# Kernel optimization log

Measured on AMD Instinct MI355X. Metric: run time of the kernel, lower is better.

The kernel has to match this reference:

```python
import jax, jax.numpy as jnp
import numpy as np

B, S, E, H = 1, 2048, 4096, 32
D = E // H
MAX_POS = 2048
NEG_MASK = -66504.0
SCALE = float(np.sqrt(D))


def _rope(x, position_ids):
    # x: [B, S, H, D]; GPT-NeoX style rotate-half rotary embedding
    half = D // 2
    inv_freq = 1.0 / (10000.0 ** (jnp.arange(0, half, dtype=jnp.float32) * 2.0 / D))  # [D/2]
    ang = position_ids.astype(jnp.float32)[:, None] * inv_freq[None, :]               # [S, D/2]
    cos = jnp.cos(ang)[None, :, None, :]
    sin = jnp.sin(ang)[None, :, None, :]
    x1, x2 = x[..., :half], x[..., half:]
    return jnp.concatenate([x1 * cos - x2 * sin, x2 * cos + x1 * sin], axis=-1)


def setup_inputs() -> dict:
    key = jax.random.key(0)
    ks = jax.random.split(key, 9)
    s = 0.02
    return {
        "hidden_states": jax.random.normal(ks[0], (B, S, E), jnp.float32),
        "wq": jax.random.normal(ks[1], (E, E), jnp.float32) * s,
        "bq": jnp.zeros((E,), jnp.float32),
        "wk": jax.random.normal(ks[2], (E, E), jnp.float32) * s,
        "bk": jnp.zeros((E,), jnp.float32),
        "wv": jax.random.normal(ks[3], (E, E), jnp.float32) * s,
        "bv": jnp.zeros((E,), jnp.float32),
        "wo": jax.random.normal(ks[4], (E, E), jnp.float32) * s,
        "bo": jnp.zeros((E,), jnp.float32),
        "position_ids": jnp.arange(S, dtype=jnp.int32),
    }


def reference(hidden_states, wq, bq, wk, bk, wv, bv, wo, bo, position_ids):
    # QKV projections (nn.Linear: x @ W.T + b)
    q = hidden_states @ wq.T + bq
    k = hidden_states @ wk.T + bk
    v = hidden_states @ wv.T + bv
    # [B, S, H, D]
    q = q.reshape(B, S, H, D)
    k = k.reshape(B, S, H, D)
    v = v.reshape(B, S, H, D)
    # rotary embedding on key and query
    q = _rope(q, position_ids)
    k = _rope(k, position_ids)
    # [B, H, S, D]
    q = q.transpose(0, 2, 1, 3)
    k = k.transpose(0, 2, 1, 3)
    v = v.transpose(0, 2, 1, 3)
    # attention scores; causal mask added BEFORE dividing by scale (faithful to source)
    scores = jnp.einsum("bhqd,bhkd->bhqk", q, k)
    causal = (1.0 - jnp.tril(jnp.ones((S, S), jnp.float32))) * NEG_MASK  # [S, S]
    scores = (scores + causal[None, None]) / SCALE
    attn = jax.nn.softmax(scores.astype(jnp.float32), axis=-1).astype(q.dtype)
    ctx = jnp.einsum("bhqk,bhkd->bhqd", attn, v)
    ctx = ctx.transpose(0, 2, 1, 3).reshape(B, S, E)
    return ctx @ wo.T + bo
```

## Files before the change

### kernel.cpp

```cpp
#include <hip/hip_runtime.h>
#include <hip/hip_bf16.h>

constexpr int SEQ = 2048;
constexpr int EMB = 4096;
constexpr int NH  = 32;
constexpr int HD  = 128;
constexpr int HALF = 64;

typedef __bf16 bf16x8 __attribute__((ext_vector_type(8)));
typedef float  f32x4  __attribute__((ext_vector_type(4)));
using u16 = unsigned short;
typedef u16 ushort8 __attribute__((ext_vector_type(8)));
typedef u16 u16x4 __attribute__((ext_vector_type(4)));

__device__ inline float bf2f(u16 u) {
  union { unsigned int i; float f; } v; v.i = ((unsigned int)u) << 16; return v.f;
}
__device__ inline u16 f2bf(float f) {
  union { __bf16 b; u16 u; } v; v.b = (__bf16)f; return v.u;
}

#define GLL16(gp, lp) __builtin_amdgcn_global_load_lds( \
    (const __attribute__((address_space(1))) void*)(gp), \
    (__attribute__((address_space(3))) void*)(lp), 16, 0, 0)

__global__ void k_f32_to_bf16(const float* __restrict__ in, u16* __restrict__ out, int n) {
  int i = (blockIdx.x * blockDim.x + threadIdx.x) * 8;
  if (i >= n) return;
  f32x4 a = *(const f32x4*)(in + i);
  f32x4 b = *(const f32x4*)(in + i + 4);
  ushort8 o;
  o[0] = f2bf(a[0]); o[1] = f2bf(a[1]); o[2] = f2bf(a[2]); o[3] = f2bf(a[3]);
  o[4] = f2bf(b[0]); o[5] = f2bf(b[1]); o[6] = f2bf(b[2]); o[7] = f2bf(b[3]);
  *(ushort8*)(out + i) = o;
}

__global__ void k_rope_table(const int* __restrict__ pos, float* __restrict__ tab) {
  int idx = blockIdx.x * blockDim.x + threadIdx.x;
  if (idx >= SEQ * HALF) return;
  int s = idx >> 6, d = idx & 63;
  double invf = pow(10000.0, -(double)d / 64.0);
  double ang = (double)pos[s] * invf;
  tab[idx * 2]     = (float)cos(ang);
  tab[idx * 2 + 1] = (float)sin(ang);
}

__global__ void k_rope(u16* __restrict__ X, const float* __restrict__ tab, float scale) {
  int idx = blockIdx.x * blockDim.x + threadIdx.x;
  if (idx >= SEQ * NH * HALF) return;
  int d = idx & 63;
  int h = (idx >> 6) & 31;
  int s = idx >> 11;
  u16* p = X + (size_t)s * EMB + h * HD + d;
  float x1 = bf2f(p[0]), x2 = bf2f(p[HALF]);
  float c  = tab[(s * HALF + d) * 2];
  float sn = tab[(s * HALF + d) * 2 + 1];
  p[0]    = f2bf((x1 * c - x2 * sn) * scale);
  p[HALF] = f2bf((x2 * c + x1 * sn) * scale);
}

template<int TBM, int TBN, int WM, int WN>
__global__ __launch_bounds__(WM * WN * 64) void k_gemm(
    const u16* __restrict__ A, const u16* __restrict__ W,
    const float* __restrict__ b0, const float* __restrict__ b1, const float* __restrict__ b2,
    void* __restrict__ C0, void* __restrict__ C1, void* __restrict__ C2,
    int M, int N, int K, int mode)
{
  constexpr int CH_A = TBM / 16, CH_B = TBN / 16;
  constexpr int CH_W = (CH_A + CH_B) / (WM * WN);
  constexpr int MA = TBM / WM / 16, NB = TBN / WN / 16;
  __shared__ alignas(16) u16 As[2][TBM * 32];
  __shared__ alignas(16) u16 Bs[2][TBN * 32];
  int tid = threadIdx.x;
  int lane = tid & 63, wid = tid >> 6;
  int wm = wid / WN, wn = wid % WN;
  int l15 = lane & 15, lhi = lane >> 4;

  int NBY = M / TBM, NBX = N / TBN;
  int wg = blockIdx.x;
  int xcd = wg & 7, s = wg >> 3;
  int by = s % NBY, bxl = s / NBY;
  int bx = xcd * (NBX >> 3) + bxl;
  int m0 = by * TBM, n0 = bx * TBN;

  f32x4 acc[MA][NB] = {};

  int srow = lane >> 2;
  int scol = (lane & 3) * 8;

  auto stage = [&](int buf, int k0) {
#pragma unroll
    for (int i = 0; i < CH_W; i++) {
      int chunk = wid * CH_W + i;
      if (chunk < CH_A) {
        int row = chunk * 16 + srow;
        GLL16(A + (size_t)(m0 + row) * K + k0 + scol, &As[buf][chunk * 512]);
      } else {
        int c2 = chunk - CH_A;
        int row = c2 * 16 + srow;
        GLL16(W + (size_t)(n0 + row) * K + k0 + scol, &Bs[buf][c2 * 512]);
      }
    }
  };

  int KT = K / 32;
  stage(0, 0);
  for (int t = 0; t < KT; t++) {
    __syncthreads();
    if (t + 1 < KT) stage((t + 1) & 1, (t + 1) * 32);

    const u16* as = As[t & 1];
    const u16* bs = Bs[t & 1];
    bf16x8 af[MA], bfr[NB];
#pragma unroll
    for (int a = 0; a < MA; a++)
      af[a] = *(const bf16x8*)&as[(wm * (TBM / WM) + a * 16 + l15) * 32 + lhi * 8];
#pragma unroll
    for (int b = 0; b < NB; b++)
      bfr[b] = *(const bf16x8*)&bs[(wn * (TBN / WN) + b * 16 + l15) * 32 + lhi * 8];
#pragma unroll
    for (int a = 0; a < MA; a++)
#pragma unroll
      for (int b = 0; b < NB; b++)
        acc[a][b] = __builtin_amdgcn_mfma_f32_16x16x32_bf16(af[a], bfr[b], acc[a][b], 0, 0, 0);
  }

  const float* bias = b0;
  void* Cout = C0;
  int mode_l = mode, Nn = N, n_base = n0;
  if (mode == 3) {
    int seg = n0 >> 12;
    Nn = EMB; n_base = n0 & 4095;
    if (seg == 0)      { bias = b0; Cout = C0; mode_l = 0; }
    else if (seg == 1) { bias = b1; Cout = C1; mode_l = 0; }
    else               { bias = b2; Cout = C2; mode_l = 2; }
  }

#pragma unroll
  for (int a = 0; a < MA; a++) {
    int m = m0 + wm * (TBM / WM) + a * 16 + lhi * 4;
#pragma unroll
    for (int b = 0; b < NB; b++) {
      int n = n_base + wn * (TBN / WN) + b * 16 + l15;
      float bs2 = bias[n];
      if (mode_l == 2) {
        u16x4 pk;
#pragma unroll
        for (int r = 0; r < 4; r++) pk[r] = f2bf(acc[a][b][r] + bs2);
        *(u16x4*)&((u16*)Cout)[(size_t)n * M + m] = pk;
      } else if (mode_l == 1) {
#pragma unroll
        for (int r = 0; r < 4; r++)
          ((float*)Cout)[(size_t)(m + r) * Nn + n] = acc[a][b][r] + bs2;
      } else {
#pragma unroll
        for (int r = 0; r < 4; r++)
          ((u16*)Cout)[(size_t)(m + r) * Nn + n] = f2bf(acc[a][b][r] + bs2);
      }
    }
  }
}

constexpr int QB = 64, KVB = 64;

__global__ __launch_bounds__(256) void k_flash(
    const u16* __restrict__ Q, const u16* __restrict__ K, const u16* __restrict__ VT,
    u16* __restrict__ ctx)
{
  __shared__ alignas(16) u16 Ks[2][KVB * 128];
  __shared__ alignas(16) u16 Vt[2][HD * 64];
  __shared__ alignas(16) u16 Pl[4][16 * 64];

  int tid = threadIdx.x, lane = tid & 63, wid = tid >> 6;
  int l15 = lane & 15, lhi = lane >> 4;
  int h = blockIdx.y;

  auto stage = [&](int buf, int t2) {
    int kv = t2 * KVB;
#pragma unroll
    for (int it = 0; it < 4; it++) {
      int chunk = tid + it * 256;
      int r = chunk >> 4, bp = chunk & 15;
      GLL16(K + (size_t)(kv + r) * EMB + h * HD + (((bp - r) & 15) << 3), &Ks[buf][chunk * 8]);
    }
#pragma unroll
    for (int it = 0; it < 4; it++) {
      int chunk = tid + it * 256;
      int d = chunk >> 3, bp = chunk & 7;
      GLL16(VT + (size_t)(h * HD + d) * SEQ + kv + (((bp - d) & 7) << 3), &Vt[buf][chunk * 8]);
    }
  };

  for (int pi = 0; pi < 2; pi++) {
    int qb = pi ? (int)blockIdx.x : 31 - (int)blockIdx.x;
    int q0 = qb * QB;
    int qw = q0 + wid * 16;

    bf16x8 qf[4];
#pragma unroll
    for (int kc = 0; kc < 4; kc++)
      qf[kc] = *(const bf16x8*)&Q[(size_t)(qw + l15) * EMB + h * HD + kc * 32 + lhi * 8];

    f32x4 O[8] = {};
    float mrow[4], lrow[4];
#pragma unroll
    for (int r = 0; r < 4; r++) { mrow[r] = -3.0e38f; lrow[r] = 0.f; }

    int nt = qb + 1;
    __syncthreads();
    stage(0, 0);
    for (int t = 0; t < nt; t++) {
      __syncthreads();
      if (t + 1 < nt) stage((t + 1) & 1, t + 1);

      const u16* ks = Ks[t & 1];
      const u16* vt = Vt[t & 1];
      float p[4][4];
      bool need_mask = (t == nt - 1);
#pragma unroll
      for (int c = 0; c < 4; c++) {
        f32x4 s = {};
        int r0 = c * 16 + l15;
#pragma unroll
        for (int kc = 0; kc < 4; kc++) {
          bf16x8 kf = *(const bf16x8*)&ks[r0 * 128 + (((kc * 4 + lhi) + r0) & 15) * 8];
          s = __builtin_amdgcn_mfma_f32_16x16x32_bf16(qf[kc], kf, s, 0, 0, 0);
        }
#pragma unroll
        for (int r = 0; r < 4; r++) {
          float sv = s[r];
          if (need_mask) {
            int qg = qw + lhi * 4 + r;
            int kg = t * KVB + c * 16 + l15;
            if (kg > qg) sv = -3.0e38f;
          }
          p[c][r] = sv;
        }
      }
      float fscale[4];
#pragma unroll
      for (int r = 0; r < 4; r++) {
        float m = fmaxf(fmaxf(p[0][r], p[1][r]), fmaxf(p[2][r], p[3][r]));
#pragma unroll
        for (int x = 1; x < 16; x <<= 1) m = fmaxf(m, __shfl_xor(m, x, 64));
        float mnew = fmaxf(mrow[r], m);
        fscale[r] = __expf(mrow[r] - mnew);
        mrow[r] = mnew;
      }
#pragma unroll
      for (int c = 0; c < 4; c++)
#pragma unroll
        for (int r = 0; r < 4; r++)
          p[c][r] = __expf(p[c][r] - mrow[r]);
#pragma unroll
      for (int r = 0; r < 4; r++) {
        float s = p[0][r] + p[1][r] + p[2][r] + p[3][r];
#pragma unroll
        for (int x = 1; x < 16; x <<= 1) s += __shfl_xor(s, x, 64);
        lrow[r] = lrow[r] * fscale[r] + s;
      }
#pragma unroll
      for (int d = 0; d < 8; d++)
#pragma unroll
        for (int r = 0; r < 4; r++)
          O[d][r] *= fscale[r];
#pragma unroll
      for (int c = 0; c < 4; c++) {
        int kb = c * 2 + (l15 >> 3), klo = l15 & 7;
#pragma unroll
        for (int r = 0; r < 4; r++) {
          int q = lhi * 4 + r;
          Pl[wid][q * 64 + ((kb + (q >> 1)) & 7) * 8 + klo] = f2bf(p[c][r]);
        }
      }
#pragma unroll
      for (int ks2 = 0; ks2 < 2; ks2++) {
        int kb = ks2 * 4 + lhi;
        bf16x8 pf = *(const bf16x8*)&Pl[wid][l15 * 64 + ((kb + (l15 >> 1)) & 7) * 8];
#pragma unroll
        for (int ds = 0; ds < 8; ds++) {
          int d = ds * 16 + l15;
          bf16x8 vf = *(const bf16x8*)&vt[d * 64 + ((kb + d) & 7) * 8];
          O[ds] = __builtin_amdgcn_mfma_f32_16x16x32_bf16(pf, vf, O[ds], 0, 0, 0);
        }
      }
    }

#pragma unroll
    for (int r = 0; r < 4; r++) {
      float inv = 1.f / lrow[r];
      int qg = q0 + wid * 16 + lhi * 4 + r;
#pragma unroll
      for (int ds = 0; ds < 8; ds++)
        ctx[(size_t)qg * EMB + h * HD + ds * 16 + l15] = f2bf(O[ds][r] * inv);
    }
  }
}

extern "C" void kernel_launch(void* const* d_in, const int* in_sizes, int n_in,
                              void* d_out, int out_size, void* d_ws, size_t ws_size,
                              hipStream_t stream) {
  const float* hs = (const float*)d_in[0];
  const float* wq = (const float*)d_in[1];
  const float* bq = (const float*)d_in[2];
  const float* wk = (const float*)d_in[3];
  const float* bk = (const float*)d_in[4];
  const float* wv = (const float*)d_in[5];
  const float* bv = (const float*)d_in[6];
  const float* wo = (const float*)d_in[7];
  const float* bo = (const float*)d_in[8];
  const int*  pos = (const int*)d_in[9];

  const size_t SE = (size_t)SEQ * EMB;
  const size_t EE = (size_t)EMB * EMB;
  const float qscale = 1.0f / 11.313708498984761f;

  char* ws = (char*)d_ws;
  size_t off = 0;
  auto alloc = [&](size_t b) { size_t o = off; off += (b + 255) & ~(size_t)255; return o; };

  size_t need_fused = ((SE * 2 + 255) & ~255ULL) + ((EE * 6 + 255) & ~255ULL) +
                      3 * ((SE * 2 + 255) & ~255ULL) + ((size_t)SEQ * HALF * 8 + 255);
  bool fused = ws_size >= need_fused + 4096;

  u16*  hsb = (u16*)(ws + alloc(SE * 2));
  u16*  wb  = (u16*)(ws + alloc(fused ? EE * 6 : EE * 2));
  u16*  Qb  = (u16*)(ws + alloc(SE * 2));
  u16*  Kb  = (u16*)(ws + alloc(SE * 2));
  u16*  VTb = (u16*)(ws + alloc(SE * 2));
  float* tab = (float*)(ws + alloc((size_t)SEQ * HALF * 2 * 4));
  u16*  ctxb = hsb;

  dim3 cb(256);
  k_f32_to_bf16<<<dim3(SE / 2048), cb, 0, stream>>>(hs, hsb, (int)SE);
  k_rope_table<<<dim3(SEQ * HALF / 256), cb, 0, stream>>>(pos, tab);

  if (fused) {
    k_f32_to_bf16<<<dim3(EE / 2048), cb, 0, stream>>>(wq, wb, (int)EE);
    k_f32_to_bf16<<<dim3(EE / 2048), cb, 0, stream>>>(wk, wb + EE, (int)EE);
    k_f32_to_bf16<<<dim3(EE / 2048), cb, 0, stream>>>(wv, wb + 2 * EE, (int)EE);
    k_gemm<128, 256, 2, 4><<<dim3(768), dim3(512), 0, stream>>>(
        hsb, wb, bq, bk, bv, (void*)Qb, (void*)Kb, (void*)VTb, SEQ, 3 * EMB, EMB, 3);
  } else {
    k_f32_to_bf16<<<dim3(EE / 2048), cb, 0, stream>>>(wq, wb, (int)EE);
    k_gemm<128, 256, 2, 4><<<dim3(256), dim3(512), 0, stream>>>(
        hsb, wb, bq, bq, bq, (void*)Qb, nullptr, nullptr, SEQ, EMB, EMB, 0);
    k_f32_to_bf16<<<dim3(EE / 2048), cb, 0, stream>>>(wk, wb, (int)EE);
    k_gemm<128, 256, 2, 4><<<dim3(256), dim3(512), 0, stream>>>(
        hsb, wb, bk, bk, bk, (void*)Kb, nullptr, nullptr, SEQ, EMB, EMB, 0);
    k_f32_to_bf16<<<dim3(EE / 2048), cb, 0, stream>>>(wv, wb, (int)EE);
    k_gemm<128, 256, 2, 4><<<dim3(256), dim3(512), 0, stream>>>(
        hsb, wb, bv, bv, bv, (void*)VTb, nullptr, nullptr, SEQ, EMB, EMB, 2);
  }

  k_rope<<<dim3(SEQ * NH * HALF / 256), cb, 0, stream>>>(Qb, tab, qscale);
  k_rope<<<dim3(SEQ * NH * HALF / 256), cb, 0, stream>>>(Kb, tab, 1.0f);

  k_flash<<<dim3(16, NH), cb, 0, stream>>>(Qb, Kb, VTb, ctxb);

  k_f32_to_bf16<<<dim3(EE / 2048), cb, 0, stream>>>(wo, wb, (int)EE);
  k_gemm<64, 128, 2, 2><<<dim3(1024), cb, 0, stream>>>(
      ctxb, wb, bo, bo, bo, d_out, nullptr, nullptr, SEQ, EMB, EMB, 1);
}
```

Measured before the change: 553.5 us.

## Replace templated GEMM with triple-buffered swizzled 128x256 BK64 kernel

Swaps the double-buffered BK=32 templated GEMM for a dedicated 128x256 tile kernel with BK=64, a three-stage LDS ring and explicit vmcnt waits. The next-next stage loads are interleaved with the MFMA sub-steps. LDS rows are XOR-style swizzled to avoid bank conflicts, and s_setprio is raised around the MFMA bursts. The output projection now also uses the large tile, at 256 workgroups instead of 1024, trading occupancy and wave count for more data reuse and fewer barriers.

```diff
diff --git a/kernel.cpp b/kernel.cpp
--- a/kernel.cpp
+++ b/kernel.cpp
@@ -59,70 +59,94 @@
   p[HALF] = f2bf((x2 * c + x1 * sn) * scale);
 }
 
-template<int TBM, int TBN, int WM, int WN>
-__global__ __launch_bounds__(WM * WN * 64) void k_gemm(
-    const u16* __restrict__ A, const u16* __restrict__ W,
+__global__ __launch_bounds__(512) void k_gemm8(
+    const u16* __restrict__ Ag, const u16* __restrict__ Wg,
     const float* __restrict__ b0, const float* __restrict__ b1, const float* __restrict__ b2,
     void* __restrict__ C0, void* __restrict__ C1, void* __restrict__ C2,
     int M, int N, int K, int mode)
 {
-  constexpr int CH_A = TBM / 16, CH_B = TBN / 16;
-  constexpr int CH_W = (CH_A + CH_B) / (WM * WN);
-  constexpr int MA = TBM / WM / 16, NB = TBN / WN / 16;
-  __shared__ alignas(16) u16 As[2][TBM * 32];
-  __shared__ alignas(16) u16 Bs[2][TBN * 32];
+  __shared__ alignas(16) u16 As[3][128 * 64];
+  __shared__ alignas(16) u16 Bs[3][256 * 64];
+
   int tid = threadIdx.x;
   int lane = tid & 63, wid = tid >> 6;
-  int wm = wid / WN, wn = wid % WN;
+  int wm = wid >> 2, wn = wid & 3;
   int l15 = lane & 15, lhi = lane >> 4;
 
-  int NBY = M / TBM, NBX = N / TBN;
+  int NBY = M / 128, NBX = N / 256;
   int wg = blockIdx.x;
-  int xcd = wg & 7, s = wg >> 3;
-  int by = s % NBY, bxl = s / NBY;
+  int xcd = wg & 7, sgl = wg >> 3;
+  int by = sgl % NBY, bxl = sgl / NBY;
   int bx = xcd * (NBX >> 3) + bxl;
-  int m0 = by * TBM, n0 = bx * TBN;
-
-  f32x4 acc[MA][NB] = {};
-
-  int srow = lane >> 2;
-  int scol = (lane & 3) * 8;
-
-  auto stage = [&](int buf, int k0) {
-#pragma unroll
-    for (int i = 0; i < CH_W; i++) {
-      int chunk = wid * CH_W + i;
-      if (chunk < CH_A) {
-        int row = chunk * 16 + srow;
-        GLL16(A + (size_t)(m0 + row) * K + k0 + scol, &As[buf][chunk * 512]);
-      } else {
-        int c2 = chunk - CH_A;
-        int row = c2 * 16 + srow;
-        GLL16(W + (size_t)(n0 + row) * K + k0 + scol, &Bs[buf][c2 * 512]);
-      }
+  int m0 = by * 128, n0 = bx * 256;
+
+  auto stageA = [&](int b, int k0) {
+#pragma unroll
+    for (int s2 = 0; s2 < 2; s2++) {
+      int row = s2 * 64 + (tid >> 3);
+      int kb = ((tid & 7) - row) & 7;
+      GLL16(Ag + (size_t)(m0 + row) * K + k0 + kb * 8, &As[b][s2 * 4096 + tid * 8]);
     }
   };
-
-  int KT = K / 32;
-  stage(0, 0);
+  auto stageBh = [&](int b, int k0, int h) {
+#pragma unroll
+    for (int s2 = 0; s2 < 2; s2++) {
+      int row = h * 128 + s2 * 64 + (tid >> 3);
+      int kb = ((tid & 7) - row) & 7;
+      GLL16(Wg + (size_t)(n0 + row) * K + k0 + kb * 8, &Bs[b][h * 8192 + s2 * 4096 + tid * 8]);
+    }
+  };
+
+  f32x4 acc[4][4] = {};
+  int KT = K >> 6;
+
+  stageA(0, 0);  stageBh(0, 0, 0);  stageBh(0, 0, 1);
+  stageA(1, 64); stageBh(1, 64, 0); stageBh(1, 64, 1);
+
   for (int t = 0; t < KT; t++) {
-    __syncthreads();
-    if (t + 1 < KT) stage((t + 1) & 1, (t + 1) * 32);
-
-    const u16* as = As[t & 1];
-    const u16* bs = Bs[t & 1];
-    bf16x8 af[MA], bfr[NB];
-#pragma unroll
-    for (int a = 0; a < MA; a++)
-      af[a] = *(const bf16x8*)&as[(wm * (TBM / WM) + a * 16 + l15) * 32 + lhi * 8];
-#pragma unroll
-    for (int b = 0; b < NB; b++)
-      bfr[b] = *(const bf16x8*)&bs[(wn * (TBN / WN) + b * 16 + l15) * 32 + lhi * 8];
-#pragma unroll
-    for (int a = 0; a < MA; a++)
-#pragma unroll
-      for (int b = 0; b < NB; b++)
-        acc[a][b] = __builtin_amdgcn_mfma_f32_16x16x32_bf16(af[a], bfr[b], acc[a][b], 0, 0, 0);
+    if (t + 1 < KT) asm volatile("s_waitcnt vmcnt(6)" ::: "memory");
+    else            asm volatile("s_waitcnt vmcnt(0)" ::: "memory");
+    __builtin_amdgcn_s_barrier();
+
+    const u16* as = &As[t % 3][0];
+    const u16* bs = &Bs[t % 3][0];
+    bool do_stage = (t + 2) < KT;
+    int bstage = (t + 2) % 3;
+    int ks = (t + 2) << 6;
+
+    bf16x8 bfr[4][2];
+#pragma unroll
+    for (int p = 0; p < 4; p++) {
+      if (p == 0) {
+#pragma unroll
+        for (int q = 0; q < 4; q++)
+#pragma unroll
+          for (int kk = 0; kk < 2; kk++) {
+            int row = wn * 64 + q * 16 + l15;
+            int pb = (kk * 4 + lhi + row) & 7;
+            bfr[q][kk] = *(const bf16x8*)&bs[row * 64 + pb * 8];
+          }
+      }
+      bf16x8 af[2];
+#pragma unroll
+      for (int kk = 0; kk < 2; kk++) {
+        int row = wm * 64 + p * 16 + l15;
+        int pb = (kk * 4 + lhi + row) & 7;
+        af[kk] = *(const bf16x8*)&as[row * 64 + pb * 8];
+      }
+      if (do_stage) {
+        if (p == 0)      stageA(bstage, ks);
+        else if (p == 1) stageBh(bstage, ks, 0);
+        else if (p == 2) stageBh(bstage, ks, 1);
+      }
+      __builtin_amdgcn_s_setprio(1);
+#pragma unroll
+      for (int q = 0; q < 4; q++)
+#pragma unroll
+        for (int kk = 0; kk < 2; kk++)
+          acc[p][q] = __builtin_amdgcn_mfma_f32_16x16x32_bf16(af[kk], bfr[q][kk], acc[p][q], 0, 0, 0);
+      __builtin_amdgcn_s_setprio(0);
+    }
   }
 
   const float* bias = b0;
@@ -137,25 +161,25 @@
   }
 
 #pragma unroll
-  for (int a = 0; a < MA; a++) {
-    int m = m0 + wm * (TBM / WM) + a * 16 + lhi * 4;
-#pragma unroll
-    for (int b = 0; b < NB; b++) {
-      int n = n_base + wn * (TBN / WN) + b * 16 + l15;
+  for (int p = 0; p < 4; p++) {
+    int m = m0 + wm * 64 + p * 16 + lhi * 4;
+#pragma unroll
+    for (int q = 0; q < 4; q++) {
+      int n = n_base + wn * 64 + q * 16 + l15;
       float bs2 = bias[n];
       if (mode_l == 2) {
         u16x4 pk;
 #pragma unroll
-        for (int r = 0; r < 4; r++) pk[r] = f2bf(acc[a][b][r] + bs2);
+        for (int r = 0; r < 4; r++) pk[r] = f2bf(acc[p][q][r] + bs2);
         *(u16x4*)&((u16*)Cout)[(size_t)n * M + m] = pk;
       } else if (mode_l == 1) {
 #pragma unroll
         for (int r = 0; r < 4; r++)
-          ((float*)Cout)[(size_t)(m + r) * Nn + n] = acc[a][b][r] + bs2;
+          ((float*)Cout)[(size_t)(m + r) * Nn + n] = acc[p][q][r] + bs2;
       } else {
 #pragma unroll
         for (int r = 0; r < 4; r++)
-          ((u16*)Cout)[(size_t)(m + r) * Nn + n] = f2bf(acc[a][b][r] + bs2);
+          ((u16*)Cout)[(size_t)(m + r) * Nn + n] = f2bf(acc[p][q][r] + bs2);
       }
     }
   }
@@ -339,17 +363,17 @@
     k_f32_to_bf16<<<dim3(EE / 2048), cb, 0, stream>>>(wq, wb, (int)EE);
     k_f32_to_bf16<<<dim3(EE / 2048), cb, 0, stream>>>(wk, wb + EE, (int)EE);
     k_f32_to_bf16<<<dim3(EE / 2048), cb, 0, stream>>>(wv, wb + 2 * EE, (int)EE);
-    k_gemm<128, 256, 2, 4><<<dim3(768), dim3(512), 0, stream>>>(
+    k_gemm8<<<dim3(768), dim3(512), 0, stream>>>(
         hsb, wb, bq, bk, bv, (void*)Qb, (void*)Kb, (void*)VTb, SEQ, 3 * EMB, EMB, 3);
   } else {
     k_f32_to_bf16<<<dim3(EE / 2048), cb, 0, stream>>>(wq, wb, (int)EE);
-    k_gemm<128, 256, 2, 4><<<dim3(256), dim3(512), 0, stream>>>(
+    k_gemm8<<<dim3(256), dim3(512), 0, stream>>>(
         hsb, wb, bq, bq, bq, (void*)Qb, nullptr, nullptr, SEQ, EMB, EMB, 0);
     k_f32_to_bf16<<<dim3(EE / 2048), cb, 0, stream>>>(wk, wb, (int)EE);
-    k_gemm<128, 256, 2, 4><<<dim3(256), dim3(512), 0, stream>>>(
+    k_gemm8<<<dim3(256), dim3(512), 0, stream>>>(
         hsb, wb, bk, bk, bk, (void*)Kb, nullptr, nullptr, SEQ, EMB, EMB, 0);
     k_f32_to_bf16<<<dim3(EE / 2048), cb, 0, stream>>>(wv, wb, (int)EE);
-    k_gemm<128, 256, 2, 4><<<dim3(256), dim3(512), 0, stream>>>(
+    k_gemm8<<<dim3(256), dim3(512), 0, stream>>>(
         hsb, wb, bv, bv, bv, (void*)VTb, nullptr, nullptr, SEQ, EMB, EMB, 2);
   }
 
@@ -359,6 +383,6 @@
   k_flash<<<dim3(16, NH), cb, 0, stream>>>(Qb, Kb, VTb, ctxb);
 
   k_f32_to_bf16<<<dim3(EE / 2048), cb, 0, stream>>>(wo, wb, (int)EE);
-  k_gemm<64, 128, 2, 2><<<dim3(1024), cb, 0, stream>>>(
+  k_gemm8<<<dim3(256), dim3(512), 0, stream>>>(
       ctxb, wb, bo, bo, bo, d_out, nullptr, nullptr, SEQ, EMB, EMB, 1);
 }
```

Result: slower. 581.4 us (+5.0%).

## Add dedicated 256x256 QKV GEMM kernel with 4-stage LDS pipeline and swizzle

Applied to the files above, without the earlier changes.

Replaces the fused QKV projection GEMM with a specialized kernel using 256x256 tiles, a 4-deep LDS ring buffer with explicit vmcnt waits, an XOR-style swizzled LDS layout to avoid bank conflicts, and loads interleaved with MFMA blocks under raised wave priority. The aim is to hide global load latency and raise MFMA utilization in the largest GEMM of the pipeline. The generic GEMM is simplified to drop the fused mode. The much larger LDS footprint (128 KB per block) and 128 accumulator registers may limit occupancy. It also halves the grid to 384 workgroups, which is fewer than two per CU.

```diff
diff --git a/kernel.cpp b/kernel.cpp
--- a/kernel.cpp
+++ b/kernel.cpp
@@ -59,12 +59,136 @@
   p[HALF] = f2bf((x2 * c + x1 * sn) * scale);
 }
 
+__global__ __launch_bounds__(512, 2) void k_qkv(
+    const u16* __restrict__ Ag, const u16* __restrict__ Wg,
+    const float* __restrict__ b0, const float* __restrict__ b1, const float* __restrict__ b2,
+    void* __restrict__ C0, void* __restrict__ C1, void* __restrict__ C2,
+    int M, int N, int K)
+{
+  __shared__ alignas(16) u16 As[4][256 * 32];
+  __shared__ alignas(16) u16 Bs[4][256 * 32];
+
+  int tid = threadIdx.x;
+  int lane = tid & 63, wid = tid >> 6;
+  int wm = wid >> 2, wn = wid & 3;
+  int l15 = lane & 15, lhi = lane >> 4;
+
+  int NBY = M >> 8, NBX = N >> 8;
+  int wg = blockIdx.x;
+  int xcd = wg & 7, sgl = wg >> 3;
+  int by = sgl % NBY, bxl = sgl / NBY;
+  int bx = xcd * (NBX >> 3) + bxl;
+  int m0 = by * 256, n0 = bx * 256;
+
+  auto stageA = [&](int b, int k0) {
+#pragma unroll
+    for (int ld = 0; ld < 2; ld++) {
+      int idx = ld * 512 + tid;
+      int row = idx >> 2, pb = idx & 3;
+      int kb = (pb - row) & 3;
+      GLL16(Ag + (size_t)(m0 + row) * K + k0 + kb * 8, &As[b][idx * 8]);
+    }
+  };
+  auto stageB = [&](int b, int k0) {
+#pragma unroll
+    for (int ld = 0; ld < 2; ld++) {
+      int idx = ld * 512 + tid;
+      int row = idx >> 2, pb = idx & 3;
+      int kb = (pb - row) & 3;
+      GLL16(Wg + (size_t)(n0 + row) * K + k0 + kb * 8, &Bs[b][idx * 8]);
+    }
+  };
+
+  f32x4 acc[8][4] = {};
+  int KT = K >> 5;
+
+  stageA(0, 0);  stageB(0, 0);
+  stageA(1, 32); stageB(1, 32);
+  stageA(2, 64); stageB(2, 64);
+
+  for (int t = 0; t < KT; t++) {
+    if (t < KT - 2)       asm volatile("s_waitcnt vmcnt(8)" ::: "memory");
+    else if (t == KT - 2) asm volatile("s_waitcnt vmcnt(4)" ::: "memory");
+    else                  asm volatile("s_waitcnt vmcnt(0)" ::: "memory");
+    __builtin_amdgcn_s_barrier();
+    __builtin_amdgcn_sched_barrier(0);
+
+    const u16* as = &As[t & 3][0];
+    const u16* bs = &Bs[t & 3][0];
+    bool st = (t + 3) < KT;
+    int sb = (t + 3) & 3, sk = (t + 3) << 5;
+
+    bf16x8 bfr[4], afA[4];
+#pragma unroll
+    for (int q = 0; q < 4; q++) {
+      int row = wn * 64 + q * 16 + l15;
+      bfr[q] = *(const bf16x8*)&bs[row * 32 + ((lhi + row) & 3) * 8];
+    }
+#pragma unroll
+    for (int p = 0; p < 4; p++) {
+      int row = wm * 128 + p * 16 + l15;
+      afA[p] = *(const bf16x8*)&as[row * 32 + ((lhi + row) & 3) * 8];
+    }
+    if (st) stageA(sb, sk);
+    asm volatile("s_waitcnt lgkmcnt(0)" ::: "memory");
+    __builtin_amdgcn_sched_barrier(0);
+    __builtin_amdgcn_s_setprio(1);
+#pragma unroll
+    for (int p = 0; p < 4; p++)
+#pragma unroll
+      for (int q = 0; q < 4; q++)
+        acc[p][q] = __builtin_amdgcn_mfma_f32_16x16x32_bf16(afA[p], bfr[q], acc[p][q], 0, 0, 0);
+    __builtin_amdgcn_s_setprio(0);
+
+    bf16x8 afB[4];
+#pragma unroll
+    for (int p = 0; p < 4; p++) {
+      int row = wm * 128 + 64 + p * 16 + l15;
+      afB[p] = *(const bf16x8*)&as[row * 32 + ((lhi + row) & 3) * 8];
+    }
+    if (st) stageB(sb, sk);
+    asm volatile("s_waitcnt lgkmcnt(0)" ::: "memory");
+    __builtin_amdgcn_sched_barrier(0);
+    __builtin_amdgcn_s_setprio(1);
+#pragma unroll
+    for (int p = 0; p < 4; p++)
+#pragma unroll
+      for (int q = 0; q < 4; q++)
+        acc[4 + p][q] = __builtin_amdgcn_mfma_f32_16x16x32_bf16(afB[p], bfr[q], acc[4 + p][q], 0, 0, 0);
+    __builtin_amdgcn_s_setprio(0);
+  }
+
+  int seg = n0 >> 12;
+  int n_base = n0 & 4095;
+  const float* bias = (seg == 0) ? b0 : (seg == 1) ? b1 : b2;
+  void* Cout = (seg == 0) ? C0 : (seg == 1) ? C1 : C2;
+
+#pragma unroll
+  for (int p = 0; p < 8; p++) {
+    int m = m0 + wm * 128 + p * 16 + lhi * 4;
+#pragma unroll
+    for (int q = 0; q < 4; q++) {
+      int n = n_base + wn * 64 + q * 16 + l15;
+      float bs2 = bias[n];
+      if (seg == 2) {
+        u16x4 pk;
+#pragma unroll
+        for (int r = 0; r < 4; r++) pk[r] = f2bf(acc[p][q][r] + bs2);
+        *(u16x4*)&((u16*)Cout)[(size_t)n * M + m] = pk;
+      } else {
+#pragma unroll
+        for (int r = 0; r < 4; r++)
+          ((u16*)Cout)[(size_t)(m + r) * EMB + n] = f2bf(acc[p][q][r] + bs2);
+      }
+    }
+  }
+}
+
 template<int TBM, int TBN, int WM, int WN>
 __global__ __launch_bounds__(WM * WN * 64) void k_gemm(
     const u16* __restrict__ A, const u16* __restrict__ W,
-    const float* __restrict__ b0, const float* __restrict__ b1, const float* __restrict__ b2,
-    void* __restrict__ C0, void* __restrict__ C1, void* __restrict__ C2,
-    int M, int N, int K, int mode)
+    const float* __restrict__ b0,
+    void* __restrict__ C0, int M, int N, int K, int mode)
 {
   constexpr int CH_A = TBM / 16, CH_B = TBN / 16;
   constexpr int CH_W = (CH_A + CH_B) / (WM * WN);
@@ -78,15 +202,13 @@
 
   int NBY = M / TBM, NBX = N / TBN;
   int wg = blockIdx.x;
-  int xcd = wg & 7, s = wg >> 3;
-  int by = s % NBY, bxl = s / NBY;
+  int xcd = wg & 7, sgl = wg >> 3;
+  int by = sgl % NBY, bxl = sgl / NBY;
   int bx = xcd * (NBX >> 3) + bxl;
   int m0 = by * TBM, n0 = bx * TBN;
 
   f32x4 acc[MA][NB] = {};
-
-  int srow = lane >> 2;
-  int scol = (lane & 3) * 8;
+  int srow = lane >> 2, scol = (lane & 3) * 8;
 
   auto stage = [&](int buf, int k0) {
 #pragma unroll
@@ -125,37 +247,26 @@
         acc[a][b] = __builtin_amdgcn_mfma_f32_16x16x32_bf16(af[a], bfr[b], acc[a][b], 0, 0, 0);
   }
 
-  const float* bias = b0;
-  void* Cout = C0;
-  int mode_l = mode, Nn = N, n_base = n0;
-  if (mode == 3) {
-    int seg = n0 >> 12;
-    Nn = EMB; n_base = n0 & 4095;
-    if (seg == 0)      { bias = b0; Cout = C0; mode_l = 0; }
-    else if (seg == 1) { bias = b1; Cout = C1; mode_l = 0; }
-    else               { bias = b2; Cout = C2; mode_l = 2; }
-  }
-
 #pragma unroll
   for (int a = 0; a < MA; a++) {
     int m = m0 + wm * (TBM / WM) + a * 16 + lhi * 4;
 #pragma unroll
     for (int b = 0; b < NB; b++) {
-      int n = n_base + wn * (TBN / WN) + b * 16 + l15;
-      float bs2 = bias[n];
-      if (mode_l == 2) {
+      int n = n0 + wn * (TBN / WN) + b * 16 + l15;
+      float bs2 = b0[n];
+      if (mode == 2) {
         u16x4 pk;
 #pragma unroll
         for (int r = 0; r < 4; r++) pk[r] = f2bf(acc[a][b][r] + bs2);
-        *(u16x4*)&((u16*)Cout)[(size_t)n * M + m] = pk;
-      } else if (mode_l == 1) {
+        *(u16x4*)&((u16*)C0)[(size_t)n * M + m] = pk;
+      } else if (mode == 1) {
 #pragma unroll
         for (int r = 0; r < 4; r++)
-          ((float*)Cout)[(size_t)(m + r) * Nn + n] = acc[a][b][r] + bs2;
+          ((float*)C0)[(size_t)(m + r) * N + n] = acc[a][b][r] + bs2;
       } else {
 #pragma unroll
         for (int r = 0; r < 4; r++)
-          ((u16*)Cout)[(size_t)(m + r) * Nn + n] = f2bf(acc[a][b][r] + bs2);
+          ((u16*)C0)[(size_t)(m + r) * N + n] = f2bf(acc[a][b][r] + bs2);
       }
     }
   }
@@ -339,18 +450,18 @@
     k_f32_to_bf16<<<dim3(EE / 2048), cb, 0, stream>>>(wq, wb, (int)EE);
     k_f32_to_bf16<<<dim3(EE / 2048), cb, 0, stream>>>(wk, wb + EE, (int)EE);
     k_f32_to_bf16<<<dim3(EE / 2048), cb, 0, stream>>>(wv, wb + 2 * EE, (int)EE);
-    k_gemm<128, 256, 2, 4><<<dim3(768), dim3(512), 0, stream>>>(
-        hsb, wb, bq, bk, bv, (void*)Qb, (void*)Kb, (void*)VTb, SEQ, 3 * EMB, EMB, 3);
+    k_qkv<<<dim3(384), dim3(512), 0, stream>>>(
+        hsb, wb, bq, bk, bv, (void*)Qb, (void*)Kb, (void*)VTb, SEQ, 3 * EMB, EMB);
   } else {
     k_f32_to_bf16<<<dim3(EE / 2048), cb, 0, stream>>>(wq, wb, (int)EE);
     k_gemm<128, 256, 2, 4><<<dim3(256), dim3(512), 0, stream>>>(
-        hsb, wb, bq, bq, bq, (void*)Qb, nullptr, nullptr, SEQ, EMB, EMB, 0);
+        hsb, wb, bq, (void*)Qb, SEQ, EMB, EMB, 0);
     k_f32_to_bf16<<<dim3(EE / 2048), cb, 0, stream>>>(wk, wb, (int)EE);
     k_gemm<128, 256, 2, 4><<<dim3(256), dim3(512), 0, stream>>>(
-        hsb, wb, bk, bk, bk, (void*)Kb, nullptr, nullptr, SEQ, EMB, EMB, 0);
+        hsb, wb, bk, (void*)Kb, SEQ, EMB, EMB, 0);
     k_f32_to_bf16<<<dim3(EE / 2048), cb, 0, stream>>>(wv, wb, (int)EE);
     k_gemm<128, 256, 2, 4><<<dim3(256), dim3(512), 0, stream>>>(
-        hsb, wb, bv, bv, bv, (void*)VTb, nullptr, nullptr, SEQ, EMB, EMB, 2);
+        hsb, wb, bv, (void*)VTb, SEQ, EMB, EMB, 2);
   }
 
   k_rope<<<dim3(SEQ * NH * HALF / 256), cb, 0, stream>>>(Qb, tab, qscale);
@@ -360,5 +471,5 @@
 
   k_f32_to_bf16<<<dim3(EE / 2048), cb, 0, stream>>>(wo, wb, (int)EE);
   k_gemm<64, 128, 2, 2><<<dim3(1024), cb, 0, stream>>>(
-      ctxb, wb, bo, bo, bo, d_out, nullptr, nullptr, SEQ, EMB, EMB, 1);
-}
+      ctxb, wb, bo, d_out, SEQ, EMB, EMB, 1);
+}
```

After: 520.3 us. -6.0%, faster.
